# Optimization experiments

Hardware: AMD Instinct MI355X
Metric: run time of the kernel (lower is better)

The kernel has to match this reference:

```python
import jax, jax.numpy as jnp
import numpy as np

STUDENT_TEMP = 0.1
CENTER_MOMENTUM = 0.9
N_CROPS = 8
GLOBAL_CROPS = 2
TOPK = 8
WARMUP_TEACHER_TEMP = 0.04
TEACHER_TEMP = 0.07
WARMUP_EPOCHS = 30
NEPOCHS = 100
B = 256          # per-crop batch
D = 8192         # out_dim


def setup_inputs() -> dict:
    key = jax.random.key(0)
    k1, k2, k3, k4 = jax.random.split(key, 4)
    return {
        "student_output": jax.random.normal(k1, (N_CROPS * B, D), jnp.float32),
        "teacher_output": jax.random.normal(k2, (GLOBAL_CROPS * B, D), jnp.float32),
        "predictor_table": 0.02 * jax.random.normal(k3, (D, D), jnp.float32),
        "center": 0.1 * jax.random.normal(k4, (1, D), jnp.float32),
        "epoch": 35,
    }


def reference(student_output, teacher_output, predictor_table, center, epoch):
    # teacher temperature schedule (static, epoch is a Python int)
    temps = np.concatenate([
        np.linspace(WARMUP_TEACHER_TEMP, TEACHER_TEMP, WARMUP_EPOCHS),
        np.ones(NEPOCHS - WARMUP_EPOCHS) * TEACHER_TEMP,
    ])
    temp = float(temps[epoch])

    # student/teacher softmaxes, chunked per crop
    student_probs = jax.nn.softmax(student_output / STUDENT_TEMP, axis=-1)
    s_chunks = jnp.split(student_probs, N_CROPS, axis=0)          # n_crops x [B, D]
    teacher_probs = jax.nn.softmax((teacher_output - center) / temp, axis=-1)
    t_chunks = jnp.split(teacher_probs, GLOBAL_CROPS, axis=0)     # global_crops x [B, D]

    # pairwise topk-weighted cross entropy
    total_loss = jnp.float32(0.0)
    n_loss_terms = 0
    for iq in range(GLOBAL_CROPS):
        for v in range(N_CROPS):
            if v <= iq:
                continue
            s = t_chunks[iq]                                       # [B, D] teacher probs
            f = s_chunks[v]                                        # [B, D] student probs
            p, indices = jax.lax.top_k(s, TOPK)                    # [B, K]
            p = p / jnp.sum(p, axis=-1, keepdims=True)
            pred = predictor_table[indices] / STUDENT_TEMP         # [B, K, D] gather
            logp = jax.nn.log_softmax(pred, axis=-1)               # [B, K, D]
            # -sum_k sum_d p[b,k] * f[b,d] * logp[b,k,d]  (outer-product weighting)
            loss_b = -jnp.einsum('bk,bd,bkd->b', p, f, logp)
            total_loss = total_loss + loss_b.mean()
            n_loss_terms += 1
    total_loss = total_loss / n_loss_terms

    # EMA center update (no-grad in original; world_size = 1)
    t_ng = jax.lax.stop_gradient(teacher_output)
    batch_center = jnp.mean(t_ng, axis=0, keepdims=True)           # [1, D]
    new_center = center * CENTER_MOMENTUM + batch_center * (1.0 - CENTER_MOMENTUM)

    log_sm_center = jax.nn.log_softmax(center, axis=-1)
    true_entropy = jnp.sum(jax.nn.softmax(center, axis=-1) * log_sm_center, axis=-1)
    entropy = jnp.sum(jax.nn.softmax(batch_center, axis=-1) * log_sm_center, axis=-1)

    return (total_loss, entropy, true_entropy, new_center)
```

## Files before the change

kernel.cpp:

```cpp
#include <hip/hip_runtime.h>
#include <hip/hip_bf16.h>
#include <math.h>

#define D 8192
#define NT 256

__device__ __forceinline__ float wave_sum(float v) {
    #pragma unroll
    for (int o = 32; o > 0; o >>= 1) v += __shfl_xor(v, o, 64);
    return v;
}

__global__ __launch_bounds__(NT) void k_topk(
    const float* __restrict__ teacher, const float* __restrict__ center,
    const int* __restrict__ epoch_p,
    int* __restrict__ idx_ws, float* __restrict__ p_ws, float* __restrict__ out)
{
    const int row = blockIdx.x;
    const int t = threadIdx.x;
    const int lane = t & 63, w = t >> 6;
    __shared__ float svv[8][4];
    __shared__ int   sii[8][4];

    if (row == 0 && t == 0) out[0] = 0.f;

    const int e = epoch_p[0];
    const float temp = (e < 30) ? (0.04f + 0.03f * (float)e / 29.0f) : 0.07f;

    float z[32];
    const float* trow = teacher + (size_t)row * D;
    #pragma unroll
    for (int i = 0; i < 8; ++i) {
        const int d = i * 1024 + t * 4;
        float4 tv = *(const float4*)(trow + d);
        float4 cv = *(const float4*)(center + d);
        z[i*4+0] = tv.x - cv.x; z[i*4+1] = tv.y - cv.y;
        z[i*4+2] = tv.z - cv.z; z[i*4+3] = tv.w - cv.w;
    }

    float mvl = -INFINITY; int mil = 0;
    #pragma unroll
    for (int i = 0; i < 32; ++i)
        if (z[i] > mvl) { mvl = z[i]; mil = i; }

    float topv[8]; int topd[8];
    #pragma unroll 1
    for (int k = 0; k < 8; ++k) {
        float mv = mvl;
        int md = ((mil >> 2) << 10) + t * 4 + (mil & 3);
        #pragma unroll
        for (int o = 32; o > 0; o >>= 1) {
            float ov = __shfl_xor(mv, o, 64);
            int   od = __shfl_xor(md, o, 64);
            if (ov > mv) { mv = ov; md = od; }
        }
        if (lane == 0) { svv[k][w] = mv; sii[k][w] = md; }
        __syncthreads();
        float gv = svv[k][0]; int gd = sii[k][0];
        #pragma unroll
        for (int j = 1; j < 4; ++j)
            if (svv[k][j] > gv) { gv = svv[k][j]; gd = sii[k][j]; }
        topv[k] = gv; topd[k] = gd;
        if (((gd & 1023) >> 2) == t) {
            z[((gd >> 10) << 2) | (gd & 3)] = -INFINITY;
            mvl = -INFINITY; mil = 0;
            #pragma unroll
            for (int i = 0; i < 32; ++i)
                if (z[i] > mvl) { mvl = z[i]; mil = i; }
        }
    }

    if (t == 0) {
        float wgt[8]; float norm = 0.f;
        #pragma unroll
        for (int k = 0; k < 8; ++k) { wgt[k] = __expf((topv[k] - topv[0]) / temp); norm += wgt[k]; }
        const float invn = 1.0f / norm;
        #pragma unroll
        for (int k = 0; k < 8; ++k) {
            p_ws[row * 8 + k] = wgt[k] * invn;
            idx_ws[row * 8 + k] = topd[k];
        }
    }
}

__global__ __launch_bounds__(NT) void k_gather_colsum(
    const float* __restrict__ pred, const int* __restrict__ idx_ws,
    const float* __restrict__ p_ws, const float* __restrict__ teacher,
    float* __restrict__ g_ws, float* __restrict__ part_lse, float* __restrict__ part)
{
    const int bid = blockIdx.x;
    const int t = threadIdx.x;

    if (bid >= 2048) {
        const int cb = bid - 2048;
        const int rc = cb >> 3, dc = cb & 7;
        const int d0 = dc * 1024 + t * 4;
        const float* base = teacher + (size_t)rc * 32 * D + d0;
        float4 acc = make_float4(0.f, 0.f, 0.f, 0.f);
        #pragma unroll 4
        for (int r = 0; r < 32; ++r) {
            float4 x = *(const float4*)(base + (size_t)r * D);
            acc.x += x.x; acc.y += x.y; acc.z += x.z; acc.w += x.w;
        }
        *(float4*)(part + (size_t)rc * D + d0) = acc;
        return;
    }

    const int row = bid >> 2;
    const int ch  = bid & 3;
    const int lane = t & 63, w = t >> 6;
    const int d0 = ch * 2048 + t * 4;
    __shared__ float sred[4][8];

    int jk[8]; float pk[8];
    #pragma unroll
    for (int k = 0; k < 8; ++k) {
        jk[k] = idx_ws[row * 8 + k];
        pk[k] = p_ws[row * 8 + k];
    }

    float4 a0 = make_float4(0.f,0.f,0.f,0.f), a1 = make_float4(0.f,0.f,0.f,0.f);
    float se[8];
    #pragma unroll
    for (int k = 0; k < 8; ++k) {
        const float* prow = pred + (size_t)jk[k] * D;
        float4 x0 = *(const float4*)(prow + d0);
        float4 x1 = *(const float4*)(prow + d0 + 1024);
        se[k] = __expf(x0.x*10.f) + __expf(x0.y*10.f) + __expf(x0.z*10.f) + __expf(x0.w*10.f)
              + __expf(x1.x*10.f) + __expf(x1.y*10.f) + __expf(x1.z*10.f) + __expf(x1.w*10.f);
        const float p = pk[k];
        a0.x += p*x0.x; a0.y += p*x0.y; a0.z += p*x0.z; a0.w += p*x0.w;
        a1.x += p*x1.x; a1.y += p*x1.y; a1.z += p*x1.z; a1.w += p*x1.w;
    }
    float* grow = g_ws + (size_t)row * D;
    *(float4*)(grow + d0)        = a0;
    *(float4*)(grow + d0 + 1024) = a1;

    #pragma unroll
    for (int k = 0; k < 8; ++k) se[k] = wave_sum(se[k]);
    if (lane == 0) {
        #pragma unroll
        for (int k = 0; k < 8; ++k) sred[w][k] = se[k];
    }
    __syncthreads();
    if (t < 8)
        part_lse[(size_t)bid * 8 + t] =
            sred[0][t] + sred[1][t] + sred[2][t] + sred[3][t];
}

__global__ __launch_bounds__(NT) void k_main(
    const float* __restrict__ student, const float* __restrict__ g_ws,
    const float* __restrict__ p_ws, const float* __restrict__ part_lse,
    const float* __restrict__ part, const float* __restrict__ center,
    float* __restrict__ ps_ws, float* __restrict__ out)
{
    const int bid = blockIdx.x;
    const int t = threadIdx.x;
    const int lane = t & 63, w = t >> 6;

    if (bid < 2) {
        __shared__ float sm4[4];
        const int r = (bid << 8) | t;
        float c = 0.f;
        #pragma unroll
        for (int k = 0; k < 8; ++k) {
            float s = part_lse[(size_t)(r*4+0)*8+k] + part_lse[(size_t)(r*4+1)*8+k]
                    + part_lse[(size_t)(r*4+2)*8+k] + part_lse[(size_t)(r*4+3)*8+k];
            c += p_ws[r * 8 + k] * __logf(s);
        }
        const float wgt = (bid == 0) ? 7.0f : 6.0f;
        float vv = wave_sum(c * wgt * (1.0f / 3328.0f));
        if (lane == 0) sm4[w] = vv;
        __syncthreads();
        if (t == 0) atomicAdd(out, sm4[0] + sm4[1] + sm4[2] + sm4[3]);
        return;
    }

    if (bid == 2) {
        __shared__ float sm4[4];
        float c[32], bc[32];
        #pragma unroll
        for (int i = 0; i < 8; ++i) {
            const int d = i * 1024 + t * 4;
            float4 cv = *(const float4*)(center + d);
            float4 s = make_float4(0.f, 0.f, 0.f, 0.f);
            for (int rc = 0; rc < 16; ++rc) {
                float4 p = *(const float4*)(part + (size_t)rc * D + d);
                s.x += p.x; s.y += p.y; s.z += p.z; s.w += p.w;
            }
            const float sc = 1.0f / 512.0f;
            bc[i*4+0] = s.x * sc; bc[i*4+1] = s.y * sc;
            bc[i*4+2] = s.z * sc; bc[i*4+3] = s.w * sc;
            c[i*4+0] = cv.x; c[i*4+1] = cv.y; c[i*4+2] = cv.z; c[i*4+3] = cv.w;
            out[3 + d + 0] = cv.x * 0.9f + bc[i*4+0] * 0.1f;
            out[3 + d + 1] = cv.y * 0.9f + bc[i*4+1] * 0.1f;
            out[3 + d + 2] = cv.z * 0.9f + bc[i*4+2] * 0.1f;
            out[3 + d + 3] = cv.w * 0.9f + bc[i*4+3] * 0.1f;
        }

        float mc = -INFINITY, mb = -INFINITY;
        #pragma unroll
        for (int i = 0; i < 32; ++i) { mc = fmaxf(mc, c[i]); mb = fmaxf(mb, bc[i]); }
        #pragma unroll
        for (int o = 32; o > 0; o >>= 1) {
            mc = fmaxf(mc, __shfl_xor(mc, o, 64));
            mb = fmaxf(mb, __shfl_xor(mb, o, 64));
        }
        if (lane == 0) sm4[w] = mc;
        __syncthreads();
        mc = fmaxf(fmaxf(sm4[0], sm4[1]), fmaxf(sm4[2], sm4[3]));
        __syncthreads();
        if (lane == 0) sm4[w] = mb;
        __syncthreads();
        mb = fmaxf(fmaxf(sm4[0], sm4[1]), fmaxf(sm4[2], sm4[3]));
        __syncthreads();

        float zc = 0.f, zb = 0.f;
        #pragma unroll
        for (int i = 0; i < 32; ++i) { zc += __expf(c[i] - mc); zb += __expf(bc[i] - mb); }
        zc = wave_sum(zc); zb = wave_sum(zb);
        if (lane == 0) sm4[w] = zc;
        __syncthreads();
        zc = sm4[0] + sm4[1] + sm4[2] + sm4[3];
        __syncthreads();
        if (lane == 0) sm4[w] = zb;
        __syncthreads();
        zb = sm4[0] + sm4[1] + sm4[2] + sm4[3];
        __syncthreads();
        const float lnZc = __logf(zc);

        float te = 0.f, en = 0.f;
        #pragma unroll
        for (int i = 0; i < 32; ++i) {
            const float lsm = c[i] - mc - lnZc;
            te += __expf(c[i] - mc) * lsm;
            en += __expf(bc[i] - mb) * lsm;
        }
        te = wave_sum(te); en = wave_sum(en);
        if (lane == 0) sm4[w] = te;
        __syncthreads();
        te = sm4[0] + sm4[1] + sm4[2] + sm4[3];
        __syncthreads();
        if (lane == 0) sm4[w] = en;
        __syncthreads();
        en = sm4[0] + sm4[1] + sm4[2] + sm4[3];
        if (t == 0) {
            out[1] = en / zb;
            out[2] = te / zc;
        }
        return;
    }

    __shared__ float sred21[4][21];
    const int sb = bid - 3;
    const int b = sb >> 2, ch = sb & 3;
    const int d0 = ch * 2048 + t * 4;

    const float* g0p = g_ws + (size_t)b * D + d0;
    const float* g1p = g_ws + (size_t)(256 + b) * D + d0;
    const float4 g0a = *(const float4*)(g0p);
    const float4 g0b = *(const float4*)(g0p + 1024);
    const float4 g1a = *(const float4*)(g1p);
    const float4 g1b = *(const float4*)(g1p + 1024);

    float accZ[7], accA0[7], accA1[7];
    #pragma unroll
    for (int vi = 0; vi < 7; ++vi) { accZ[vi] = 0.f; accA0[vi] = 0.f; accA1[vi] = 0.f; }

    #pragma unroll
    for (int vi = 0; vi < 7; ++vi) {
        const int row = 256 * (vi + 1) + b;
        const float* sp = student + (size_t)row * D + d0;
        float4 x0 = *(const float4*)(sp);
        float4 x1 = *(const float4*)(sp + 1024);
        float y0 = __expf(x0.x*10.f), y1 = __expf(x0.y*10.f);
        float y2 = __expf(x0.z*10.f), y3 = __expf(x0.w*10.f);
        float y4 = __expf(x1.x*10.f), y5 = __expf(x1.y*10.f);
        float y6 = __expf(x1.z*10.f), y7 = __expf(x1.w*10.f);
        accZ[vi]  = y0+y1+y2+y3+y4+y5+y6+y7;
        accA0[vi] = y0*g0a.x + y1*g0a.y + y2*g0a.z + y3*g0a.w
                  + y4*g0b.x + y5*g0b.y + y6*g0b.z + y7*g0b.w;
        accA1[vi] = y0*g1a.x + y1*g1a.y + y2*g1a.z + y3*g1a.w
                  + y4*g1b.x + y5*g1b.y + y6*g1b.z + y7*g1b.w;
    }

    #pragma unroll
    for (int vi = 0; vi < 7; ++vi) {
        accZ[vi]  = wave_sum(accZ[vi]);
        accA0[vi] = wave_sum(accA0[vi]);
        accA1[vi] = wave_sum(accA1[vi]);
    }
    if (lane == 0) {
        #pragma unroll
        for (int vi = 0; vi < 7; ++vi) {
            sred21[w][vi*3+0] = accZ[vi];
            sred21[w][vi*3+1] = accA0[vi];
            sred21[w][vi*3+2] = accA1[vi];
        }
    }
    __syncthreads();
    if (t < 21)
        ps_ws[(size_t)sb * 24 + t] =
            sred21[0][t] + sred21[1][t] + sred21[2][t] + sred21[3][t];
}

__global__ __launch_bounds__(NT) void k_sfinal(
    const float* __restrict__ ps_ws, float* __restrict__ out)
{
    const int t = threadIdx.x;
    const int lane = t & 63, w = t >> 6;
    __shared__ float sm4[4];
    const int g = blockIdx.x * NT + t;
    const int vi = g >> 8;
    const int b  = g & 255;

    float Z = 0.f, A0 = 0.f, A1 = 0.f;
    #pragma unroll
    for (int ch = 0; ch < 4; ++ch) {
        const float* p = ps_ws + (size_t)(b * 4 + ch) * 24 + vi * 3;
        Z += p[0]; A0 += p[1]; A1 += p[2];
    }
    float term = -10.f * (A0 + ((vi >= 1) ? A1 : 0.f)) / Z;
    float vv = wave_sum(term * (1.0f / 3328.0f));
    if (lane == 0) sm4[w] = vv;
    __syncthreads();
    if (t == 0) atomicAdd(out, sm4[0] + sm4[1] + sm4[2] + sm4[3]);
}

extern "C" void kernel_launch(void* const* d_in, const int* in_sizes, int n_in,
                              void* d_out, int out_size, void* d_ws, size_t ws_size,
                              hipStream_t stream) {
    const float* student = (const float*)d_in[0];
    const float* teacher = (const float*)d_in[1];
    const float* pred    = (const float*)d_in[2];
    const float* center  = (const float*)d_in[3];
    const int*   epoch   = (const int*)d_in[4];
    float* out = (float*)d_out;

    float* g_ws     = (float*)d_ws;
    float* part     = g_ws + (size_t)512 * D;
    int*   idx_ws   = (int*)(part + (size_t)16 * D);
    float* p_ws     = (float*)(idx_ws + 512 * 8);
    float* part_lse = p_ws + 512 * 8;
    float* ps_ws    = part_lse + 2048 * 8;

    k_topk<<<512, NT, 0, stream>>>(teacher, center, epoch, idx_ws, p_ws, out);
    k_gather_colsum<<<2176, NT, 0, stream>>>(pred, idx_ws, p_ws, teacher,
                                             g_ws, part_lse, part);
    k_main<<<1027, NT, 0, stream>>>(student, g_ws, p_ws, part_lse, part, center,
                                    ps_ws, out);
    k_sfinal<<<7, NT, 0, stream>>>(ps_ws, out);
}
```

Before: 71.46 us.

## Fuse gather and student dot-products into one kernel, dropping g_ws intermediate

Each gather block now also loads the matching student rows, computes their exp values, and dots them with each gathered predictor row weighted by p. This removes the 16 MB g_ws write/read round trip and merges the old main and sfinal kernels into one small finalize kernel, cutting a launch. In exchange, student rows are read twice (once for each teacher crop) and per-thread register pressure rises from holding NV×8 exp values.

New measurement: 77.47 us. 1.08x slower.

```diff
diff --git a/kernel.cpp b/kernel.cpp
--- a/kernel.cpp
+++ b/kernel.cpp
@@ -83,10 +83,97 @@
     }
 }
 
-__global__ __launch_bounds__(NT) void k_gather_colsum(
-    const float* __restrict__ pred, const int* __restrict__ idx_ws,
-    const float* __restrict__ p_ws, const float* __restrict__ teacher,
-    float* __restrict__ g_ws, float* __restrict__ part_lse, float* __restrict__ part)
+template<int NV, int V0>
+__device__ __forceinline__ void mega_body(
+    const int r, const int ch, const int t,
+    const float* __restrict__ student, const float* __restrict__ pred,
+    const int* __restrict__ idx_ws, const float* __restrict__ p_ws,
+    float* __restrict__ part_lse, float* __restrict__ psA, float* __restrict__ psZ)
+{
+    const int lane = t & 63, w = t >> 6;
+    const int b = r & 255;
+    const int d0 = ch * 2048 + t * 4;
+    __shared__ float sred[4][24];
+
+    int jk[8]; float pk[8];
+    #pragma unroll
+    for (int k = 0; k < 8; ++k) {
+        jk[k] = idx_ws[r * 8 + k];
+        pk[k] = p_ws[r * 8 + k];
+    }
+
+    float y[NV][8];
+    #pragma unroll
+    for (int vi = 0; vi < NV; ++vi) {
+        const float* sp = student + (size_t)(256 * (V0 + vi) + b) * D + d0;
+        float4 x0 = *(const float4*)sp;
+        float4 x1 = *(const float4*)(sp + 1024);
+        y[vi][0] = __expf(x0.x*10.f); y[vi][1] = __expf(x0.y*10.f);
+        y[vi][2] = __expf(x0.z*10.f); y[vi][3] = __expf(x0.w*10.f);
+        y[vi][4] = __expf(x1.x*10.f); y[vi][5] = __expf(x1.y*10.f);
+        y[vi][6] = __expf(x1.z*10.f); y[vi][7] = __expf(x1.w*10.f);
+    }
+    float Zp[NV], acc[NV];
+    #pragma unroll
+    for (int vi = 0; vi < NV; ++vi) {
+        Zp[vi] = y[vi][0]+y[vi][1]+y[vi][2]+y[vi][3]+y[vi][4]+y[vi][5]+y[vi][6]+y[vi][7];
+        acc[vi] = 0.f;
+    }
+
+    float se[8];
+    #pragma unroll
+    for (int k = 0; k < 8; ++k) {
+        const float* prow = pred + (size_t)jk[k] * D;
+        float4 x0 = *(const float4*)(prow + d0);
+        float4 x1 = *(const float4*)(prow + d0 + 1024);
+        se[k] = __expf(x0.x*10.f) + __expf(x0.y*10.f) + __expf(x0.z*10.f) + __expf(x0.w*10.f)
+              + __expf(x1.x*10.f) + __expf(x1.y*10.f) + __expf(x1.z*10.f) + __expf(x1.w*10.f);
+        const float p = pk[k];
+        #pragma unroll
+        for (int vi = 0; vi < NV; ++vi) {
+            acc[vi] += p * (y[vi][0]*x0.x + y[vi][1]*x0.y + y[vi][2]*x0.z + y[vi][3]*x0.w
+                          + y[vi][4]*x1.x + y[vi][5]*x1.y + y[vi][6]*x1.z + y[vi][7]*x1.w);
+        }
+    }
+
+    #pragma unroll
+    for (int k = 0; k < 8; ++k) se[k] = wave_sum(se[k]);
+    #pragma unroll
+    for (int vi = 0; vi < NV; ++vi) { acc[vi] = wave_sum(acc[vi]); }
+    if constexpr (V0 == 1) {
+        #pragma unroll
+        for (int vi = 0; vi < NV; ++vi) Zp[vi] = wave_sum(Zp[vi]);
+    }
+    if (lane == 0) {
+        #pragma unroll
+        for (int k = 0; k < 8; ++k) sred[w][k] = se[k];
+        #pragma unroll
+        for (int vi = 0; vi < NV; ++vi) sred[w][8 + vi] = acc[vi];
+        if constexpr (V0 == 1) {
+            #pragma unroll
+            for (int vi = 0; vi < NV; ++vi) sred[w][15 + vi] = Zp[vi];
+        }
+    }
+    __syncthreads();
+    if (t < 8)
+        part_lse[(size_t)(r * 4 + ch) * 8 + t] =
+            sred[0][t] + sred[1][t] + sred[2][t] + sred[3][t];
+    if (t >= 8 && t < 8 + NV)
+        psA[(size_t)(b * 4 + ch) * 8 + (t - 8)] =
+            sred[0][t] + sred[1][t] + sred[2][t] + sred[3][t];
+    if constexpr (V0 == 1) {
+        if (t >= 15 && t < 22)
+            psZ[(size_t)(b * 4 + ch) * 8 + (t - 15)] =
+                sred[0][t] + sred[1][t] + sred[2][t] + sred[3][t];
+    }
+}
+
+__global__ __launch_bounds__(NT) void k_mega(
+    const float* __restrict__ student, const float* __restrict__ pred,
+    const int* __restrict__ idx_ws, const float* __restrict__ p_ws,
+    const float* __restrict__ teacher,
+    float* __restrict__ part_lse, float* __restrict__ psA0,
+    float* __restrict__ psA1, float* __restrict__ psZ, float* __restrict__ part)
 {
     const int bid = blockIdx.x;
     const int t = threadIdx.x;
@@ -106,53 +193,18 @@
         return;
     }
 
-    const int row = bid >> 2;
-    const int ch  = bid & 3;
-    const int lane = t & 63, w = t >> 6;
-    const int d0 = ch * 2048 + t * 4;
-    __shared__ float sred[4][8];
-
-    int jk[8]; float pk[8];
-    #pragma unroll
-    for (int k = 0; k < 8; ++k) {
-        jk[k] = idx_ws[row * 8 + k];
-        pk[k] = p_ws[row * 8 + k];
-    }
-
-    float4 a0 = make_float4(0.f,0.f,0.f,0.f), a1 = make_float4(0.f,0.f,0.f,0.f);
-    float se[8];
-    #pragma unroll
-    for (int k = 0; k < 8; ++k) {
-        const float* prow = pred + (size_t)jk[k] * D;
-        float4 x0 = *(const float4*)(prow + d0);
-        float4 x1 = *(const float4*)(prow + d0 + 1024);
-        se[k] = __expf(x0.x*10.f) + __expf(x0.y*10.f) + __expf(x0.z*10.f) + __expf(x0.w*10.f)
-              + __expf(x1.x*10.f) + __expf(x1.y*10.f) + __expf(x1.z*10.f) + __expf(x1.w*10.f);
-        const float p = pk[k];
-        a0.x += p*x0.x; a0.y += p*x0.y; a0.z += p*x0.z; a0.w += p*x0.w;
-        a1.x += p*x1.x; a1.y += p*x1.y; a1.z += p*x1.z; a1.w += p*x1.w;
-    }
-    float* grow = g_ws + (size_t)row * D;
-    *(float4*)(grow + d0)        = a0;
-    *(float4*)(grow + d0 + 1024) = a1;
-
-    #pragma unroll
-    for (int k = 0; k < 8; ++k) se[k] = wave_sum(se[k]);
-    if (lane == 0) {
-        #pragma unroll
-        for (int k = 0; k < 8; ++k) sred[w][k] = se[k];
-    }
-    __syncthreads();
-    if (t < 8)
-        part_lse[(size_t)bid * 8 + t] =
-            sred[0][t] + sred[1][t] + sred[2][t] + sred[3][t];
-}
-
-__global__ __launch_bounds__(NT) void k_main(
-    const float* __restrict__ student, const float* __restrict__ g_ws,
+    const int r = bid >> 2, ch = bid & 3;
+    if (r < 256)
+        mega_body<7, 1>(r, ch, t, student, pred, idx_ws, p_ws, part_lse, psA0, psZ);
+    else
+        mega_body<6, 2>(r, ch, t, student, pred, idx_ws, p_ws, part_lse, psA1, psZ);
+}
+
+__global__ __launch_bounds__(NT) void k_fin(
     const float* __restrict__ p_ws, const float* __restrict__ part_lse,
     const float* __restrict__ part, const float* __restrict__ center,
-    float* __restrict__ ps_ws, float* __restrict__ out)
+    const float* __restrict__ psA0, const float* __restrict__ psA1,
+    const float* __restrict__ psZ, float* __restrict__ out)
 {
     const int bid = blockIdx.x;
     const int t = threadIdx.x;
@@ -251,76 +303,21 @@
         return;
     }
 
-    __shared__ float sred21[4][21];
-    const int sb = bid - 3;
-    const int b = sb >> 2, ch = sb & 3;
-    const int d0 = ch * 2048 + t * 4;
-
-    const float* g0p = g_ws + (size_t)b * D + d0;
-    const float* g1p = g_ws + (size_t)(256 + b) * D + d0;
-    const float4 g0a = *(const float4*)(g0p);
-    const float4 g0b = *(const float4*)(g0p + 1024);
-    const float4 g1a = *(const float4*)(g1p);
-    const float4 g1b = *(const float4*)(g1p + 1024);
-
-    float accZ[7], accA0[7], accA1[7];
-    #pragma unroll
-    for (int vi = 0; vi < 7; ++vi) { accZ[vi] = 0.f; accA0[vi] = 0.f; accA1[vi] = 0.f; }
-
-    #pragma unroll
-    for (int vi = 0; vi < 7; ++vi) {
-        const int row = 256 * (vi + 1) + b;
-        const float* sp = student + (size_t)row * D + d0;
-        float4 x0 = *(const float4*)(sp);
-        float4 x1 = *(const float4*)(sp + 1024);
-        float y0 = __expf(x0.x*10.f), y1 = __expf(x0.y*10.f);
-        float y2 = __expf(x0.z*10.f), y3 = __expf(x0.w*10.f);
-        float y4 = __expf(x1.x*10.f), y5 = __expf(x1.y*10.f);
-        float y6 = __expf(x1.z*10.f), y7 = __expf(x1.w*10.f);
-        accZ[vi]  = y0+y1+y2+y3+y4+y5+y6+y7;
-        accA0[vi] = y0*g0a.x + y1*g0a.y + y2*g0a.z + y3*g0a.w
-                  + y4*g0b.x + y5*g0b.y + y6*g0b.z + y7*g0b.w;
-        accA1[vi] = y0*g1a.x + y1*g1a.y + y2*g1a.z + y3*g1a.w
-                  + y4*g1b.x + y5*g1b.y + y6*g1b.z + y7*g1b.w;
-    }
-
-    #pragma unroll
-    for (int vi = 0; vi < 7; ++vi) {
-        accZ[vi]  = wave_sum(accZ[vi]);
-        accA0[vi] = wave_sum(accA0[vi]);
-        accA1[vi] = wave_sum(accA1[vi]);
-    }
-    if (lane == 0) {
-        #pragma unroll
-        for (int vi = 0; vi < 7; ++vi) {
-            sred21[w][vi*3+0] = accZ[vi];
-            sred21[w][vi*3+1] = accA0[vi];
-            sred21[w][vi*3+2] = accA1[vi];
-        }
-    }
-    __syncthreads();
-    if (t < 21)
-        ps_ws[(size_t)sb * 24 + t] =
-            sred21[0][t] + sred21[1][t] + sred21[2][t] + sred21[3][t];
-}
-
-__global__ __launch_bounds__(NT) void k_sfinal(
-    const float* __restrict__ ps_ws, float* __restrict__ out)
-{
-    const int t = threadIdx.x;
-    const int lane = t & 63, w = t >> 6;
     __shared__ float sm4[4];
-    const int g = blockIdx.x * NT + t;
+    const int g = (bid - 3) * NT + t;
     const int vi = g >> 8;
     const int b  = g & 255;
+    const int v  = vi + 1;
 
     float Z = 0.f, A0 = 0.f, A1 = 0.f;
     #pragma unroll
     for (int ch = 0; ch < 4; ++ch) {
-        const float* p = ps_ws + (size_t)(b * 4 + ch) * 24 + vi * 3;
-        Z += p[0]; A0 += p[1]; A1 += p[2];
-    }
-    float term = -10.f * (A0 + ((vi >= 1) ? A1 : 0.f)) / Z;
+        const size_t base = (size_t)(b * 4 + ch) * 8;
+        Z  += psZ [base + vi];
+        A0 += psA0[base + vi];
+        if (v >= 2) A1 += psA1[base + (v - 2)];
+    }
+    const float term = -10.f * (A0 + A1) / Z;
     float vv = wave_sum(term * (1.0f / 3328.0f));
     if (lane == 0) sm4[w] = vv;
     __syncthreads();
@@ -337,17 +334,17 @@
     const int*   epoch   = (const int*)d_in[4];
     float* out = (float*)d_out;
 
-    float* g_ws     = (float*)d_ws;
-    float* part     = g_ws + (size_t)512 * D;
+    float* part     = (float*)d_ws;
     int*   idx_ws   = (int*)(part + (size_t)16 * D);
     float* p_ws     = (float*)(idx_ws + 512 * 8);
     float* part_lse = p_ws + 512 * 8;
-    float* ps_ws    = part_lse + 2048 * 8;
+    float* psA0     = part_lse + 2048 * 8;
+    float* psA1     = psA0 + 1024 * 8;
+    float* psZ      = psA1 + 1024 * 8;
 
     k_topk<<<512, NT, 0, stream>>>(teacher, center, epoch, idx_ws, p_ws, out);
-    k_gather_colsum<<<2176, NT, 0, stream>>>(pred, idx_ws, p_ws, teacher,
-                                             g_ws, part_lse, part);
-    k_main<<<1027, NT, 0, stream>>>(student, g_ws, p_ws, part_lse, part, center,
-                                    ps_ws, out);
-    k_sfinal<<<7, NT, 0, stream>>>(ps_ws, out);
-}
+    k_mega<<<2176, NT, 0, stream>>>(student, pred, idx_ws, p_ws, teacher,
+                                    part_lse, psA0, psA1, psZ, part);
+    k_fin<<<10, NT, 0, stream>>>(p_ws, part_lse, part, center,
+                                 psA0, psA1, psZ, out);
+}
```
